# Kernel optimization log

Measured on AMD Instinct MI355X. Metric: run time of the kernel, lower is better.

The kernel has to match this reference:

```python
import jax, jax.numpy as jnp
import numpy as np

THRESHOLD = 0.01


def setup_inputs() -> dict:
    key = jax.random.key(0)
    ks = jax.random.split(key, 6)
    N = 100_000      # neurons (square connectome)
    NNZ = 6_400_000  # edges, avg degree 64
    B = 8            # batch
    T = 8            # num_layers / timesteps
    S = 5_000        # sensory neurons
    G = 200          # neuron-type groups
    rows = jax.random.randint(ks[0], (NNZ,), 0, N, dtype=jnp.int32)
    cols = jax.random.randint(ks[1], (NNZ,), 0, N, dtype=jnp.int32)
    vals = jax.random.normal(ks[2], (NNZ,), jnp.float32) * 0.05
    sensory_indices = jnp.arange(S, dtype=jnp.int32)
    group_indices = jax.random.randint(ks[3], (N,), 0, G, dtype=jnp.int32)
    slope = jnp.full((G,), 5.0, jnp.float32)       # tanh_steepness default
    raw_biases = jnp.zeros((G,), jnp.float32)      # default_bias = 0.0
    inputs = jax.random.uniform(ks[4], (B, S, T), jnp.float32)
    return dict(vals=vals, rows=rows, cols=cols, sensory_indices=sensory_indices,
                group_indices=group_indices, slope=slope, raw_biases=raw_biases,
                inputs=inputs, num_neurons=N)


def _spmm(vals, rows, cols, x, n):
    # y[i, b] = sum_e vals[e] * x[cols[e], b]   (COO sparse @ dense)
    return jax.ops.segment_sum(vals[:, None] * x[cols], rows, num_segments=n)


def reference(vals, rows, cols, sensory_indices, group_indices, slope,
              raw_biases, inputs, num_neurons):
    B, S, T = inputs.shape
    n = num_neurons
    # clip sensory inputs: below threshold -> 0, above 1 -> 1
    inputs = jnp.where(inputs >= THRESHOLD, inputs, 0.0)
    inputs = jnp.minimum(inputs, 1.0)
    slopes = slope[group_indices][:, None]                     # (N, 1)
    biases = jax.nn.softplus(raw_biases)[group_indices][:, None]

    def act(x):  # tanh(threshold(slope*x + bias))
        y = slopes * x + biases
        y = jnp.where(y >= THRESHOLD, y, 0.0)
        return jnp.tanh(y)

    acts = []
    # t = 0: only external input
    full = jnp.zeros((n, B), inputs.dtype).at[sensory_indices].add(inputs[:, :, 0].T)
    x = act(_spmm(vals, rows, cols, full, n))
    acts.append(x)
    # t >= 1: internal activation + external input
    for t in range(1, T):
        full = x.at[sensory_indices].add(inputs[:, :, t].T)
        x = act(_spmm(vals, rows, cols, full, n))
        acts.append(x)
    return jnp.stack(acts, axis=2).transpose(1, 0, 2)  # (B, N, T)
```

## Files before the change

kernel.cpp:

```cpp
#include <hip/hip_runtime.h>
#include <cstdint>
#include <cstddef>

constexpr int N       = 100000;
constexpr int NNZ     = 6400000;
constexpr int B       = 8;
constexpr int T       = 8;
constexpr int S       = 5000;
constexpr int BIN1_BITS = 8;
constexpr int BIN1    = 1 << BIN1_BITS;
constexpr int NBINS1  = (N + BIN1 - 1) / BIN1;
constexpr int CHUNK   = 8192;
constexpr int NCHUNKS = (NNZ + CHUNK - 1) / CHUNK;
constexpr int STAGE_CAP = 17408;
constexpr float THRESH = 0.01f;

__device__ __forceinline__ unsigned pack_val15(unsigned fbits, unsigned col17) {
    unsigned xb = fbits + 0x1000u;
    unsigned sign = xb >> 31;
    int ex = (int)((xb >> 23) & 0xFFu) - 110;
    ex = ex < 0 ? 0 : (ex > 15 ? 15 : ex);
    unsigned u15 = (sign << 14) | ((unsigned)ex << 10) | ((xb >> 13) & 0x3FFu);
    return (col17 << 15) | u15;
}

__device__ __forceinline__ float dec_val15(unsigned w) {
    unsigned fb = ((w & 0x4000u) << 17) | ((((w >> 10) & 0xFu) + 110u) << 23)
                | ((w & 0x3FFu) << 13);
    return __uint_as_float(fb);
}

__global__ void k_precompute_sb(const int* __restrict__ gi,
                                const float* __restrict__ slope,
                                const float* __restrict__ raw_biases,
                                float* __restrict__ slopeN,
                                float* __restrict__ biasN) {
    int i = blockIdx.x * 256 + threadIdx.x;
    if (i < N) {
        int g = gi[i];
        slopeN[i] = slope[g];
        float rb = raw_biases[g];
        biasN[i] = (rb > 20.0f) ? rb : log1pf(expf(rb));
    }
}

__global__ void k_hist(const int* __restrict__ rows, unsigned* __restrict__ counts) {
    __shared__ unsigned hist[NBINS1];
    int tid = threadIdx.x, chunk = blockIdx.x;
    for (int i = tid; i < NBINS1; i += 256) hist[i] = 0;
    __syncthreads();
    int base = chunk * CHUNK;
    #pragma unroll 4
    for (int it = 0; it < CHUNK / 256; ++it) {
        int e = base + it * 256 + tid;
        if (e < NNZ) atomicAdd(&hist[((unsigned)rows[e]) >> BIN1_BITS], 1u);
    }
    __syncthreads();
    for (int i = tid; i < NBINS1; i += 256) counts[(size_t)i * NCHUNKS + chunk] = hist[i];
}

__global__ void k_scan_chunks(unsigned* __restrict__ counts, unsigned* __restrict__ binTot) {
    int bin = blockIdx.x, lane = threadIdx.x;
    unsigned carry = 0;
    for (int bse = 0; bse < NCHUNKS; bse += 64) {
        int idx = bse + lane;
        unsigned v = (idx < NCHUNKS) ? counts[(size_t)bin * NCHUNKS + idx] : 0u;
        unsigned x = v;
        #pragma unroll
        for (int off = 1; off < 64; off <<= 1) {
            unsigned y = __shfl_up(x, off, 64);
            if (lane >= off) x += y;
        }
        if (idx < NCHUNKS) counts[(size_t)bin * NCHUNKS + idx] = x - v + carry;
        carry += __shfl(x, 63, 64);
    }
    if (lane == 0) binTot[bin] = carry;
}

__global__ void k_scan_bins(const unsigned* __restrict__ binTot, unsigned* __restrict__ binBase) {
    int lane = threadIdx.x;
    unsigned carry = 0;
    for (int bse = 0; bse < NBINS1; bse += 64) {
        int idx = bse + lane;
        unsigned v = (idx < NBINS1) ? binTot[idx] : 0u;
        unsigned x = v;
        #pragma unroll
        for (int off = 1; off < 64; off <<= 1) {
            unsigned y = __shfl_up(x, off, 64);
            if (lane >= off) x += y;
        }
        if (idx < NBINS1) binBase[idx] = x - v + carry;
        carry += __shfl(x, 63, 64);
    }
    if (lane == 0) binBase[NBINS1] = carry;
}

__global__ __launch_bounds__(512)
void k_scatter(const int* __restrict__ rows, const int* __restrict__ cols,
               const float* __restrict__ vals,
               const unsigned* __restrict__ binBase,
               const unsigned* __restrict__ counts,
               uint2* __restrict__ pk) {
    __shared__ uint2    stage[CHUNK];
    __shared__ unsigned lcnt[NBINS1];
    __shared__ unsigned lofs[NBINS1 + 1];
    __shared__ unsigned gdst[NBINS1];
    int tid = threadIdx.x, chunk = blockIdx.x;
    int base = chunk * CHUNK;
    for (int i = tid; i < NBINS1; i += 512) lcnt[i] = 0;
    __syncthreads();
    for (int i = tid; i < CHUNK; i += 512) {
        int e = base + i;
        if (e < NNZ) atomicAdd(&lcnt[((unsigned)rows[e]) >> BIN1_BITS], 1u);
    }
    __syncthreads();
    if (tid < 64) {
        unsigned carry = 0;
        for (int bse = 0; bse < NBINS1; bse += 64) {
            int idx = bse + tid;
            unsigned v = (idx < NBINS1) ? lcnt[idx] : 0u;
            unsigned x = v;
            #pragma unroll
            for (int off = 1; off < 64; off <<= 1) {
                unsigned y = __shfl_up(x, off, 64);
                if (tid >= off) x += y;
            }
            if (idx < NBINS1) lofs[idx] = x - v + carry;
            carry += __shfl(x, 63, 64);
        }
        if (tid == 0) lofs[NBINS1] = carry;
    }
    __syncthreads();
    if (tid < NBINS1) {
        lcnt[tid] = lofs[tid];
        gdst[tid] = binBase[tid] + counts[(size_t)tid * NCHUNKS + chunk];
    }
    __syncthreads();
    for (int i = tid; i < CHUNK; i += 512) {
        int e = base + i;
        if (e < NNZ) {
            unsigned r = (unsigned)rows[e];
            unsigned c = (unsigned)cols[e];
            float    v = vals[e];
            unsigned b1 = r >> BIN1_BITS, lr = r & (BIN1 - 1);
            unsigned pos = atomicAdd(&lcnt[b1], 1u);
            stage[pos] = make_uint2(__float_as_uint(v), c | (lr << 17));
        }
    }
    __syncthreads();
    int wave = tid >> 6, lane = tid & 63;
    for (int b1 = wave; b1 < NBINS1; b1 += 8) {
        unsigned s = lofs[b1], epos = lcnt[b1];
        unsigned g = gdst[b1];
        for (unsigned j = s + lane; j < epos; j += 64)
            pk[(size_t)g + (j - s)] = stage[j];
    }
}

__global__ __launch_bounds__(512)
void k_sortbin(const uint2* __restrict__ pk,
               const unsigned* __restrict__ binBase,
               unsigned* __restrict__ pk2,
               unsigned* __restrict__ rowPtr) {
    __shared__ unsigned stage[STAGE_CAP];
    __shared__ unsigned cnt[BIN1];
    __shared__ unsigned ofs[BIN1];
    int tid = threadIdx.x, bin = blockIdx.x;
    if (tid < BIN1) cnt[tid] = 0;
    __syncthreads();
    unsigned s = binBase[bin], e = binBase[bin + 1];
    unsigned total = e - s;
    for (unsigned i = s + tid; i < e; i += 512)
        atomicAdd(&cnt[pk[i].y >> 17], 1u);
    __syncthreads();
    if (tid < BIN1) ofs[tid] = cnt[tid];
    __syncthreads();
    for (int off = 1; off < BIN1; off <<= 1) {
        unsigned v = (tid < BIN1 && tid >= off) ? ofs[tid - off] : 0u;
        __syncthreads();
        if (tid < BIN1) ofs[tid] += v;
        __syncthreads();
    }
    if (tid < BIN1) {
        unsigned excl = ofs[tid] - cnt[tid];
        int row = bin * BIN1 + tid;
        if (row <= N) rowPtr[row] = s + excl;
        cnt[tid] = excl;
    }
    __syncthreads();
    if (total <= (unsigned)STAGE_CAP) {
        for (unsigned i = s + tid; i < e; i += 512) {
            uint2 p = pk[i];
            unsigned w = pack_val15(p.x, p.y & 0x1FFFFu);
            unsigned pos = atomicAdd(&cnt[p.y >> 17], 1u);
            stage[pos] = w;
        }
        __syncthreads();
        for (unsigned j = tid; j < total; j += 512)
            pk2[(size_t)s + j] = stage[j];
    } else {
        for (unsigned i = s + tid; i < e; i += 512) {
            uint2 p = pk[i];
            unsigned w = pack_val15(p.x, p.y & 0x1FFFFu);
            unsigned pos = atomicAdd(&cnt[p.y >> 17], 1u);
            pk2[(size_t)s + pos] = w;
        }
    }
}

__global__ void k_sensory(const float* __restrict__ inputs, const int* __restrict__ sidx,
                          float* __restrict__ X, int t) {
    int idx = blockIdx.x * 256 + threadIdx.x;
    if (idx < S * B) {
        int s = idx >> 3, b = idx & 7;
        float val = inputs[((size_t)b * S + s) * T + t];
        val = (val >= THRESH) ? fminf(val, 1.0f) : 0.0f;
        atomicAdd(&X[(size_t)sidx[s] * B + b], val);
    }
}

__device__ __forceinline__ float wave_fold8(const float* a, int lane) {
    int l1 = lane & 1, l2 = lane & 2, l4 = lane & 4;
    float k0 = l1 ? a[1] : a[0], s0 = l1 ? a[0] : a[1];
    float k1 = l1 ? a[3] : a[2], s1 = l1 ? a[2] : a[3];
    float k2 = l1 ? a[5] : a[4], s2 = l1 ? a[4] : a[5];
    float k3 = l1 ? a[7] : a[6], s3 = l1 ? a[6] : a[7];
    k0 += __shfl_xor(s0, 1, 64);
    k1 += __shfl_xor(s1, 1, 64);
    k2 += __shfl_xor(s2, 1, 64);
    k3 += __shfl_xor(s3, 1, 64);
    float m0 = l2 ? k1 : k0, t0 = l2 ? k0 : k1;
    float m1 = l2 ? k3 : k2, t1 = l2 ? k2 : k3;
    m0 += __shfl_xor(t0, 2, 64);
    m1 += __shfl_xor(t1, 2, 64);
    float r = l4 ? m1 : m0, u = l4 ? m0 : m1;
    r += __shfl_xor(u, 4, 64);
    r += __shfl_xor(r, 8, 64);
    r += __shfl_xor(r, 16, 64);
    r += __shfl_xor(r, 32, 64);
    return r;
}

__global__ __launch_bounds__(256)
void k_step(const unsigned* __restrict__ pk2,
            const unsigned* __restrict__ rowPtr,
            const float* __restrict__ Xin,
            const float* __restrict__ slopeN,
            const float* __restrict__ biasN,
            float* __restrict__ Sout,
            float* __restrict__ Xnext,
            const float* __restrict__ inputs, int tnext, int has_next, unsigned cmax) {
    int lane = threadIdx.x & 63;
    int wv = __builtin_amdgcn_readfirstlane(blockIdx.x * 4 + (threadIdx.x >> 6));
    int r0 = wv * 4;
    if (r0 >= N) return;

    unsigned P[5];
    #pragma unroll
    for (int r = 0; r < 5; ++r) {
        int rr = r0 + r; rr = rr > N ? N : rr;
        P[r] = rowPtr[rr];
    }

    float acc[4][8];
    #pragma unroll
    for (int r = 0; r < 4; ++r)
        #pragma unroll
        for (int b = 0; b < 8; ++b) acc[r][b] = 0.f;

    unsigned w1[4], w2[4];
    bool m1[4], m2[4];
    #pragma unroll
    for (int r = 0; r < 4; ++r) {
        unsigned e = P[r] + lane;
        m1[r] = e < P[r + 1];
        w1[r] = m1[r] ? pk2[e] : 0u;
    }
    #pragma unroll
    for (int r = 0; r < 4; ++r) {
        unsigned e = P[r] + 64 + lane;
        m2[r] = e < P[r + 1];
        w2[r] = m2[r] ? pk2[e] : 0u;
    }

    #pragma unroll
    for (int it = 0; it < 2; ++it) {
        #pragma unroll
        for (int r = 0; r < 4; ++r) {
            unsigned w = it ? w2[r] : w1[r];
            bool     m = it ? m2[r] : m1[r];
            float4 x0 = make_float4(0.f, 0.f, 0.f, 0.f), x1 = x0;
            if (m && (w >> 15) < cmax) {
                const float4* fx = (const float4*)(Xin + (size_t)(w >> 15) * B);
                x0 = fx[0]; x1 = fx[1];
            }
            float v = dec_val15(w);
            acc[r][0] += v * x0.x; acc[r][1] += v * x0.y;
            acc[r][2] += v * x0.z; acc[r][3] += v * x0.w;
            acc[r][4] += v * x1.x; acc[r][5] += v * x1.y;
            acc[r][6] += v * x1.z; acc[r][7] += v * x1.w;
        }
    }

    #pragma unroll
    for (int r = 0; r < 4; ++r) {
        for (unsigned e = P[r] + 128 + lane; e < P[r + 1]; e += 64) {
            unsigned w = pk2[e];
            float4 x0 = make_float4(0.f, 0.f, 0.f, 0.f), x1 = x0;
            if ((w >> 15) < cmax) {
                const float4* fx = (const float4*)(Xin + (size_t)(w >> 15) * B);
                x0 = fx[0]; x1 = fx[1];
            }
            float v = dec_val15(w);
            acc[r][0] += v * x0.x; acc[r][1] += v * x0.y;
            acc[r][2] += v * x0.z; acc[r][3] += v * x0.w;
            acc[r][4] += v * x1.x; acc[r][5] += v * x1.y;
            acc[r][6] += v * x1.z; acc[r][7] += v * x1.w;
        }
    }

    float f0 = wave_fold8(acc[0], lane);
    float f1 = wave_fold8(acc[1], lane);
    float f2 = wave_fold8(acc[2], lane);
    float f3 = wave_fold8(acc[3], lane);

    int lr = (lane >> 3) & 3;
    int b  = lane & 7;
    int row = r0 + lr;
    int rc = row < N - 1 ? row : N - 1;
    float sl = slopeN[rc], bi = biasN[rc];
    float fs = lr == 0 ? f0 : lr == 1 ? f1 : lr == 2 ? f2 : f3;
    float y = sl * fs + bi;
    y = (y >= THRESH) ? y : 0.f;
    float o = tanhf(y);

    if (lane < 32 && row < N) {
        size_t idx = (size_t)row * B + b;
        Sout[idx] = o;
        float xn = o;
        if (has_next && row < S) {
            float val = inputs[((size_t)b * S + row) * T + tnext];
            val = (val >= THRESH) ? fminf(val, 1.0f) : 0.0f;
            xn += val;
        }
        Xnext[idx] = xn;
    }
}

__global__ __launch_bounds__(512)
void k_transpose(const float* __restrict__ St, float* __restrict__ out) {
    __shared__ float tile[64][8][9];
    int r0 = blockIdx.x * 64;
    int tid = threadIdx.x;
    int ri = tid >> 3, rb = tid & 7;
    #pragma unroll
    for (int t = 0; t < T; ++t) {
        int r = r0 + ri;
        if (r < N)
            tile[ri][t][rb] = St[(size_t)t * N * B + (size_t)r * B + rb];
    }
    __syncthreads();
    int wi = tid >> 3, wt = tid & 7;
    #pragma unroll
    for (int b = 0; b < B; ++b) {
        int r = r0 + wi;
        if (r < N)
            out[(size_t)b * N * T + (size_t)r * T + wt] = tile[wi][wt][b];
    }
}

extern "C" void kernel_launch(void* const* d_in, const int* in_sizes, int n_in,
                              void* d_out, int out_size, void* d_ws, size_t ws_size,
                              hipStream_t stream) {
    const float* vals  = (const float*)d_in[0];
    const int*   rows  = (const int*)d_in[1];
    const int*   cols  = (const int*)d_in[2];
    const int*   sidx  = (const int*)d_in[3];
    const int*   gi    = (const int*)d_in[4];
    const float* slope = (const float*)d_in[5];
    const float* rawb  = (const float*)d_in[6];
    const float* inputs = (const float*)d_in[7];
    float* out = (float*)d_out;

    char* ws = (char*)d_ws;
    uint2*    pk     = (uint2*)ws;
    float*    St     = (float*)ws;
    float*    Xin0   = (float*)(ws + 25600000);
    float*    Xin1   = (float*)(ws + 28800000);
    float*    slopeN = (float*)(ws + 32000000);
    float*    biasN  = (float*)(ws + 32400000);
    char*     wsB    = ws + 51200000;
    unsigned* pk2    = (unsigned*)wsB;
    unsigned* counts = (unsigned*)wsB;
    char*     wsC    = wsB + 25600000;
    unsigned* binTot  = (unsigned*)(wsC);
    unsigned* binBase = (unsigned*)(wsC + 4096);
    unsigned* rowPtr  = (unsigned*)(wsC + 8192);
    size_t need = 76800000 + 8192 + (size_t)(N + 1) * 4 + 256;
    if (need > ws_size) return;

    k_hist<<<NCHUNKS, 256, 0, stream>>>(rows, counts);
    k_scan_chunks<<<NBINS1, 64, 0, stream>>>(counts, binTot);
    k_scan_bins<<<1, 64, 0, stream>>>(binTot, binBase);
    k_scatter<<<NCHUNKS, 512, 0, stream>>>(rows, cols, vals, binBase, counts, pk);
    k_sortbin<<<NBINS1, 512, 0, stream>>>(pk, binBase, pk2, rowPtr);
    k_precompute_sb<<<(N + 255) / 256, 256, 0, stream>>>(gi, slope, rawb, slopeN, biasN);

    hipMemsetAsync(Xin0, 0, (size_t)N * B * 4, stream);
    k_sensory<<<(S * B + 255) / 256, 256, 0, stream>>>(inputs, sidx, Xin0, 0);

    float* Xcur = Xin0;
    float* Xnxt = Xin1;
    for (int t = 0; t < T; ++t) {
        unsigned cmax = (t == 0) ? (unsigned)S : (unsigned)N;
        k_step<<<(N + 15) / 16, 256, 0, stream>>>(
            pk2, rowPtr, Xcur, slopeN, biasN, St + (size_t)t * N * B, Xnxt,
            inputs, t + 1, (t + 1 < T) ? 1 : 0, cmax);
        float* tmp = Xcur; Xcur = Xnxt; Xnxt = tmp;
    }
    k_transpose<<<(N + 63) / 64, 512, 0, stream>>>(St, out);
}
```

Measured before the change: 403.4 us.

## Vectorize COO preprocessing loads, reuse histogram counts in scatter, flatten copy-out

Halves the chunk size, uses int4/float4 loads in both the histogram and scatter kernels, and gives each wave its own shared-memory histogram copy to cut atomic contention. The scatter kernel no longer re-counts rows. It derives per-chunk bin counts from the exclusive-scanned counts array (next chunk minus current, or binTot for the last chunk). The staged copy-out now runs as a flat loop driven by a per-entry bin index, replacing the per-wave bin loop that left lanes idle on small bins. The trade-off is twice as many blocks and more scan work over NCHUNKS, plus extra shared memory for the bin-index array.

```diff
diff --git a/kernel.cpp b/kernel.cpp
--- a/kernel.cpp
+++ b/kernel.cpp
@@ -10,7 +10,7 @@
 constexpr int BIN1_BITS = 8;
 constexpr int BIN1    = 1 << BIN1_BITS;
 constexpr int NBINS1  = (N + BIN1 - 1) / BIN1;
-constexpr int CHUNK   = 8192;
+constexpr int CHUNK   = 4096;
 constexpr int NCHUNKS = (NNZ + CHUNK - 1) / CHUNK;
 constexpr int STAGE_CAP = 17408;
 constexpr float THRESH = 0.01f;
@@ -44,19 +44,29 @@
     }
 }
 
-__global__ void k_hist(const int* __restrict__ rows, unsigned* __restrict__ counts) {
-    __shared__ unsigned hist[NBINS1];
+__global__ __launch_bounds__(256)
+void k_hist(const int* __restrict__ rows, unsigned* __restrict__ counts) {
+    __shared__ unsigned hist[4][NBINS1];
     int tid = threadIdx.x, chunk = blockIdx.x;
-    for (int i = tid; i < NBINS1; i += 256) hist[i] = 0;
-    __syncthreads();
-    int base = chunk * CHUNK;
-    #pragma unroll 4
-    for (int it = 0; it < CHUNK / 256; ++it) {
-        int e = base + it * 256 + tid;
-        if (e < NNZ) atomicAdd(&hist[((unsigned)rows[e]) >> BIN1_BITS], 1u);
-    }
-    __syncthreads();
-    for (int i = tid; i < NBINS1; i += 256) counts[(size_t)i * NCHUNKS + chunk] = hist[i];
+    int wv = tid >> 6;
+    for (int i = tid; i < 4 * NBINS1; i += 256) ((unsigned*)hist)[i] = 0;
+    __syncthreads();
+    int base4 = chunk * (CHUNK / 4);
+    #pragma unroll
+    for (int it = 0; it < CHUNK / 1024; ++it) {
+        int i4 = base4 + it * 256 + tid;
+        if (i4 * 4 < NNZ) {
+            int4 r4 = ((const int4*)rows)[i4];
+            atomicAdd(&hist[wv][((unsigned)r4.x) >> BIN1_BITS], 1u);
+            atomicAdd(&hist[wv][((unsigned)r4.y) >> BIN1_BITS], 1u);
+            atomicAdd(&hist[wv][((unsigned)r4.z) >> BIN1_BITS], 1u);
+            atomicAdd(&hist[wv][((unsigned)r4.w) >> BIN1_BITS], 1u);
+        }
+    }
+    __syncthreads();
+    for (int i = tid; i < NBINS1; i += 256)
+        counts[(size_t)i * NCHUNKS + chunk] =
+            hist[0][i] + hist[1][i] + hist[2][i] + hist[3][i];
 }
 
 __global__ void k_scan_chunks(unsigned* __restrict__ counts, unsigned* __restrict__ binTot) {
@@ -99,19 +109,23 @@
 void k_scatter(const int* __restrict__ rows, const int* __restrict__ cols,
                const float* __restrict__ vals,
                const unsigned* __restrict__ binBase,
+               const unsigned* __restrict__ binTot,
                const unsigned* __restrict__ counts,
                uint2* __restrict__ pk) {
-    __shared__ uint2    stage[CHUNK];
+    __shared__ uint2          stage[CHUNK];
+    __shared__ unsigned short bidx[CHUNK];
     __shared__ unsigned lcnt[NBINS1];
     __shared__ unsigned lofs[NBINS1 + 1];
     __shared__ unsigned gdst[NBINS1];
     int tid = threadIdx.x, chunk = blockIdx.x;
     int base = chunk * CHUNK;
-    for (int i = tid; i < NBINS1; i += 512) lcnt[i] = 0;
-    __syncthreads();
-    for (int i = tid; i < CHUNK; i += 512) {
-        int e = base + i;
-        if (e < NNZ) atomicAdd(&lcnt[((unsigned)rows[e]) >> BIN1_BITS], 1u);
+
+    for (int i = tid; i < NBINS1; i += 512) {
+        unsigned cur = counts[(size_t)i * NCHUNKS + chunk];
+        unsigned nxt = (chunk + 1 < NCHUNKS) ? counts[(size_t)i * NCHUNKS + chunk + 1]
+                                             : binTot[i];
+        lcnt[i] = nxt - cur;
+        gdst[i] = binBase[i] + cur;
     }
     __syncthreads();
     if (tid < 64) {
@@ -131,29 +145,51 @@
         if (tid == 0) lofs[NBINS1] = carry;
     }
     __syncthreads();
-    if (tid < NBINS1) {
-        lcnt[tid] = lofs[tid];
-        gdst[tid] = binBase[tid] + counts[(size_t)tid * NCHUNKS + chunk];
-    }
-    __syncthreads();
-    for (int i = tid; i < CHUNK; i += 512) {
-        int e = base + i;
-        if (e < NNZ) {
-            unsigned r = (unsigned)rows[e];
-            unsigned c = (unsigned)cols[e];
-            float    v = vals[e];
-            unsigned b1 = r >> BIN1_BITS, lr = r & (BIN1 - 1);
-            unsigned pos = atomicAdd(&lcnt[b1], 1u);
-            stage[pos] = make_uint2(__float_as_uint(v), c | (lr << 17));
-        }
-    }
-    __syncthreads();
-    int wave = tid >> 6, lane = tid & 63;
-    for (int b1 = wave; b1 < NBINS1; b1 += 8) {
-        unsigned s = lofs[b1], epos = lcnt[b1];
-        unsigned g = gdst[b1];
-        for (unsigned j = s + lane; j < epos; j += 64)
-            pk[(size_t)g + (j - s)] = stage[j];
+    if (tid < NBINS1) lcnt[tid] = lofs[tid];
+    __syncthreads();
+
+    #pragma unroll
+    for (int it = 0; it < CHUNK / 2048; ++it) {
+        int i4 = base / 4 + it * 512 + tid;
+        if (i4 * 4 < NNZ) {
+            int4   r4 = ((const int4*)rows)[i4];
+            int4   c4 = ((const int4*)cols)[i4];
+            float4 v4 = ((const float4*)vals)[i4];
+            {
+                unsigned r = (unsigned)r4.x, b1 = r >> BIN1_BITS;
+                unsigned pos = atomicAdd(&lcnt[b1], 1u);
+                stage[pos] = make_uint2(__float_as_uint(v4.x),
+                                        (unsigned)c4.x | ((r & (BIN1 - 1)) << 17));
+                bidx[pos] = (unsigned short)b1;
+            }
+            {
+                unsigned r = (unsigned)r4.y, b1 = r >> BIN1_BITS;
+                unsigned pos = atomicAdd(&lcnt[b1], 1u);
+                stage[pos] = make_uint2(__float_as_uint(v4.y),
+                                        (unsigned)c4.y | ((r & (BIN1 - 1)) << 17));
+                bidx[pos] = (unsigned short)b1;
+            }
+            {
+                unsigned r = (unsigned)r4.z, b1 = r >> BIN1_BITS;
+                unsigned pos = atomicAdd(&lcnt[b1], 1u);
+                stage[pos] = make_uint2(__float_as_uint(v4.z),
+                                        (unsigned)c4.z | ((r & (BIN1 - 1)) << 17));
+                bidx[pos] = (unsigned short)b1;
+            }
+            {
+                unsigned r = (unsigned)r4.w, b1 = r >> BIN1_BITS;
+                unsigned pos = atomicAdd(&lcnt[b1], 1u);
+                stage[pos] = make_uint2(__float_as_uint(v4.w),
+                                        (unsigned)c4.w | ((r & (BIN1 - 1)) << 17));
+                bidx[pos] = (unsigned short)b1;
+            }
+        }
+    }
+    __syncthreads();
+    unsigned total = lofs[NBINS1];
+    for (unsigned j = tid; j < total; j += 512) {
+        unsigned b = bidx[j];
+        pk[(size_t)gdst[b] + (j - lofs[b])] = stage[j];
     }
 }
 
@@ -402,7 +438,7 @@
     k_hist<<<NCHUNKS, 256, 0, stream>>>(rows, counts);
     k_scan_chunks<<<NBINS1, 64, 0, stream>>>(counts, binTot);
     k_scan_bins<<<1, 64, 0, stream>>>(binTot, binBase);
-    k_scatter<<<NCHUNKS, 512, 0, stream>>>(rows, cols, vals, binBase, counts, pk);
+    k_scatter<<<NCHUNKS, 512, 0, stream>>>(rows, cols, vals, binBase, binTot, counts, pk);
     k_sortbin<<<NBINS1, 512, 0, stream>>>(pk, binBase, pk2, rowPtr);
     k_precompute_sb<<<(N + 255) / 256, 256, 0, stream>>>(gi, slope, rawb, slopeN, biasN);
 
```

Measured after the change: 392.9 us (median of 2 runs). 1.03x faster.

## Replace two-pass binned COO-to-CSR sort with direct per-row atomic histogram and scatter

Applied to the files above, without the earlier changes.

Replaces the chunked bin histogram, shared-memory staging scatter and per-bin local sort with a global per-row atomic histogram, a three-kernel prefix scan, and a direct atomic-cursor scatter into packed CSR. This removes the intermediate 8-byte staging array and several passes over it. In exchange it issues millions of global atomics at random addresses, and it writes scattered 4-byte values, which makes the order of entries within a row nondeterministic.

```diff
diff --git a/kernel.cpp b/kernel.cpp
--- a/kernel.cpp
+++ b/kernel.cpp
@@ -7,12 +7,8 @@
 constexpr int B       = 8;
 constexpr int T       = 8;
 constexpr int S       = 5000;
-constexpr int BIN1_BITS = 8;
-constexpr int BIN1    = 1 << BIN1_BITS;
-constexpr int NBINS1  = (N + BIN1 - 1) / BIN1;
-constexpr int CHUNK   = 8192;
-constexpr int NCHUNKS = (NNZ + CHUNK - 1) / CHUNK;
-constexpr int STAGE_CAP = 17408;
+constexpr int SCAN_BT = 1024;
+constexpr int SCAN_NB = (N + SCAN_BT - 1) / SCAN_BT;
 constexpr float THRESH = 0.01f;
 
 __device__ __forceinline__ unsigned pack_val15(unsigned fbits, unsigned col17) {
@@ -44,167 +40,100 @@
     }
 }
 
-__global__ void k_hist(const int* __restrict__ rows, unsigned* __restrict__ counts) {
-    __shared__ unsigned hist[NBINS1];
-    int tid = threadIdx.x, chunk = blockIdx.x;
-    for (int i = tid; i < NBINS1; i += 256) hist[i] = 0;
+__global__ __launch_bounds__(256)
+void k_hist_row(const int* __restrict__ rows, unsigned* __restrict__ rowCnt) {
+    int i4 = blockIdx.x * 256 + threadIdx.x;
+    if (i4 * 4 < NNZ) {
+        int4 r4 = ((const int4*)rows)[i4];
+        atomicAdd(&rowCnt[(unsigned)r4.x], 1u);
+        atomicAdd(&rowCnt[(unsigned)r4.y], 1u);
+        atomicAdd(&rowCnt[(unsigned)r4.z], 1u);
+        atomicAdd(&rowCnt[(unsigned)r4.w], 1u);
+    }
+}
+
+__global__ __launch_bounds__(1024)
+void k_scanA(const unsigned* __restrict__ rowCnt, unsigned* __restrict__ rowPtr,
+             unsigned* __restrict__ blockSum) {
+    __shared__ unsigned wsum[16];
+    int tid = threadIdx.x;
+    int idx = blockIdx.x * SCAN_BT + tid;
+    unsigned v = (idx < N) ? rowCnt[idx] : 0u;
+    unsigned x = v;
+    #pragma unroll
+    for (int off = 1; off < 64; off <<= 1) {
+        unsigned y = __shfl_up(x, off, 64);
+        if ((tid & 63) >= off) x += y;
+    }
+    int wv = tid >> 6, ln = tid & 63;
+    if (ln == 63) wsum[wv] = x;
     __syncthreads();
-    int base = chunk * CHUNK;
-    #pragma unroll 4
-    for (int it = 0; it < CHUNK / 256; ++it) {
-        int e = base + it * 256 + tid;
-        if (e < NNZ) atomicAdd(&hist[((unsigned)rows[e]) >> BIN1_BITS], 1u);
+    if (tid < 16) {
+        unsigned s = wsum[tid];
+        unsigned y = s;
+        #pragma unroll
+        for (int off = 1; off < 16; off <<= 1) {
+            unsigned z = __shfl_up(y, off, 64);
+            if (tid >= off) y += z;
+        }
+        wsum[tid] = y - s;
     }
     __syncthreads();
-    for (int i = tid; i < NBINS1; i += 256) counts[(size_t)i * NCHUNKS + chunk] = hist[i];
-}
-
-__global__ void k_scan_chunks(unsigned* __restrict__ counts, unsigned* __restrict__ binTot) {
-    int bin = blockIdx.x, lane = threadIdx.x;
+    unsigned excl = x - v + wsum[wv];
+    if (idx < N) rowPtr[idx] = excl;
+    if (tid == SCAN_BT - 1) blockSum[blockIdx.x] = wsum[15] + x;
+}
+
+__global__ void k_scanB(unsigned* __restrict__ blockSum) {
+    int lane = threadIdx.x;
     unsigned carry = 0;
-    for (int bse = 0; bse < NCHUNKS; bse += 64) {
+    for (int bse = 0; bse < SCAN_NB; bse += 64) {
         int idx = bse + lane;
-        unsigned v = (idx < NCHUNKS) ? counts[(size_t)bin * NCHUNKS + idx] : 0u;
+        unsigned v = (idx < SCAN_NB) ? blockSum[idx] : 0u;
         unsigned x = v;
         #pragma unroll
         for (int off = 1; off < 64; off <<= 1) {
             unsigned y = __shfl_up(x, off, 64);
             if (lane >= off) x += y;
         }
-        if (idx < NCHUNKS) counts[(size_t)bin * NCHUNKS + idx] = x - v + carry;
+        if (idx < SCAN_NB) blockSum[idx] = x - v + carry;
         carry += __shfl(x, 63, 64);
     }
-    if (lane == 0) binTot[bin] = carry;
-}
-
-__global__ void k_scan_bins(const unsigned* __restrict__ binTot, unsigned* __restrict__ binBase) {
-    int lane = threadIdx.x;
-    unsigned carry = 0;
-    for (int bse = 0; bse < NBINS1; bse += 64) {
-        int idx = bse + lane;
-        unsigned v = (idx < NBINS1) ? binTot[idx] : 0u;
-        unsigned x = v;
-        #pragma unroll
-        for (int off = 1; off < 64; off <<= 1) {
-            unsigned y = __shfl_up(x, off, 64);
-            if (lane >= off) x += y;
-        }
-        if (idx < NBINS1) binBase[idx] = x - v + carry;
-        carry += __shfl(x, 63, 64);
-    }
-    if (lane == 0) binBase[NBINS1] = carry;
-}
-
-__global__ __launch_bounds__(512)
-void k_scatter(const int* __restrict__ rows, const int* __restrict__ cols,
-               const float* __restrict__ vals,
-               const unsigned* __restrict__ binBase,
-               const unsigned* __restrict__ counts,
-               uint2* __restrict__ pk) {
-    __shared__ uint2    stage[CHUNK];
-    __shared__ unsigned lcnt[NBINS1];
-    __shared__ unsigned lofs[NBINS1 + 1];
-    __shared__ unsigned gdst[NBINS1];
-    int tid = threadIdx.x, chunk = blockIdx.x;
-    int base = chunk * CHUNK;
-    for (int i = tid; i < NBINS1; i += 512) lcnt[i] = 0;
-    __syncthreads();
-    for (int i = tid; i < CHUNK; i += 512) {
-        int e = base + i;
-        if (e < NNZ) atomicAdd(&lcnt[((unsigned)rows[e]) >> BIN1_BITS], 1u);
-    }
-    __syncthreads();
-    if (tid < 64) {
-        unsigned carry = 0;
-        for (int bse = 0; bse < NBINS1; bse += 64) {
-            int idx = bse + tid;
-            unsigned v = (idx < NBINS1) ? lcnt[idx] : 0u;
-            unsigned x = v;
-            #pragma unroll
-            for (int off = 1; off < 64; off <<= 1) {
-                unsigned y = __shfl_up(x, off, 64);
-                if (tid >= off) x += y;
-            }
-            if (idx < NBINS1) lofs[idx] = x - v + carry;
-            carry += __shfl(x, 63, 64);
-        }
-        if (tid == 0) lofs[NBINS1] = carry;
-    }
-    __syncthreads();
-    if (tid < NBINS1) {
-        lcnt[tid] = lofs[tid];
-        gdst[tid] = binBase[tid] + counts[(size_t)tid * NCHUNKS + chunk];
-    }
-    __syncthreads();
-    for (int i = tid; i < CHUNK; i += 512) {
-        int e = base + i;
-        if (e < NNZ) {
-            unsigned r = (unsigned)rows[e];
-            unsigned c = (unsigned)cols[e];
-            float    v = vals[e];
-            unsigned b1 = r >> BIN1_BITS, lr = r & (BIN1 - 1);
-            unsigned pos = atomicAdd(&lcnt[b1], 1u);
-            stage[pos] = make_uint2(__float_as_uint(v), c | (lr << 17));
-        }
-    }
-    __syncthreads();
-    int wave = tid >> 6, lane = tid & 63;
-    for (int b1 = wave; b1 < NBINS1; b1 += 8) {
-        unsigned s = lofs[b1], epos = lcnt[b1];
-        unsigned g = gdst[b1];
-        for (unsigned j = s + lane; j < epos; j += 64)
-            pk[(size_t)g + (j - s)] = stage[j];
-    }
-}
-
-__global__ __launch_bounds__(512)
-void k_sortbin(const uint2* __restrict__ pk,
-               const unsigned* __restrict__ binBase,
-               unsigned* __restrict__ pk2,
-               unsigned* __restrict__ rowPtr) {
-    __shared__ unsigned stage[STAGE_CAP];
-    __shared__ unsigned cnt[BIN1];
-    __shared__ unsigned ofs[BIN1];
-    int tid = threadIdx.x, bin = blockIdx.x;
-    if (tid < BIN1) cnt[tid] = 0;
-    __syncthreads();
-    unsigned s = binBase[bin], e = binBase[bin + 1];
-    unsigned total = e - s;
-    for (unsigned i = s + tid; i < e; i += 512)
-        atomicAdd(&cnt[pk[i].y >> 17], 1u);
-    __syncthreads();
-    if (tid < BIN1) ofs[tid] = cnt[tid];
-    __syncthreads();
-    for (int off = 1; off < BIN1; off <<= 1) {
-        unsigned v = (tid < BIN1 && tid >= off) ? ofs[tid - off] : 0u;
-        __syncthreads();
-        if (tid < BIN1) ofs[tid] += v;
-        __syncthreads();
-    }
-    if (tid < BIN1) {
-        unsigned excl = ofs[tid] - cnt[tid];
-        int row = bin * BIN1 + tid;
-        if (row <= N) rowPtr[row] = s + excl;
-        cnt[tid] = excl;
-    }
-    __syncthreads();
-    if (total <= (unsigned)STAGE_CAP) {
-        for (unsigned i = s + tid; i < e; i += 512) {
-            uint2 p = pk[i];
-            unsigned w = pack_val15(p.x, p.y & 0x1FFFFu);
-            unsigned pos = atomicAdd(&cnt[p.y >> 17], 1u);
-            stage[pos] = w;
-        }
-        __syncthreads();
-        for (unsigned j = tid; j < total; j += 512)
-            pk2[(size_t)s + j] = stage[j];
-    } else {
-        for (unsigned i = s + tid; i < e; i += 512) {
-            uint2 p = pk[i];
-            unsigned w = pack_val15(p.x, p.y & 0x1FFFFu);
-            unsigned pos = atomicAdd(&cnt[p.y >> 17], 1u);
-            pk2[(size_t)s + pos] = w;
-        }
+}
+
+__global__ __launch_bounds__(1024)
+void k_scanC(unsigned* __restrict__ rowPtr, const unsigned* __restrict__ blockSum,
+             unsigned* __restrict__ cursors) {
+    int idx = blockIdx.x * SCAN_BT + threadIdx.x;
+    if (idx < N) {
+        unsigned p = rowPtr[idx] + blockSum[blockIdx.x];
+        rowPtr[idx]  = p;
+        cursors[idx] = p;
+    }
+    if (idx == N) rowPtr[N] = NNZ;
+}
+
+__global__ __launch_bounds__(256)
+void k_scatter_direct(const int* __restrict__ rows, const int* __restrict__ cols,
+                      const float* __restrict__ vals,
+                      unsigned* __restrict__ cursors, unsigned* __restrict__ pk2) {
+    int i4 = blockIdx.x * 256 + threadIdx.x;
+    if (i4 * 4 < NNZ) {
+        int4   r4 = ((const int4*)rows)[i4];
+        int4   c4 = ((const int4*)cols)[i4];
+        float4 v4 = ((const float4*)vals)[i4];
+        unsigned w0 = pack_val15(__float_as_uint(v4.x), (unsigned)c4.x);
+        unsigned w1 = pack_val15(__float_as_uint(v4.y), (unsigned)c4.y);
+        unsigned w2 = pack_val15(__float_as_uint(v4.z), (unsigned)c4.z);
+        unsigned w3 = pack_val15(__float_as_uint(v4.w), (unsigned)c4.w);
+        unsigned p0 = atomicAdd(&cursors[(unsigned)r4.x], 1u);
+        unsigned p1 = atomicAdd(&cursors[(unsigned)r4.y], 1u);
+        unsigned p2 = atomicAdd(&cursors[(unsigned)r4.z], 1u);
+        unsigned p3 = atomicAdd(&cursors[(unsigned)r4.w], 1u);
+        pk2[p0] = w0;
+        pk2[p1] = w1;
+        pk2[p2] = w2;
+        pk2[p3] = w3;
     }
 }
 
@@ -383,27 +312,26 @@
     float* out = (float*)d_out;
 
     char* ws = (char*)d_ws;
-    uint2*    pk     = (uint2*)ws;
-    float*    St     = (float*)ws;
-    float*    Xin0   = (float*)(ws + 25600000);
-    float*    Xin1   = (float*)(ws + 28800000);
-    float*    slopeN = (float*)(ws + 32000000);
-    float*    biasN  = (float*)(ws + 32400000);
-    char*     wsB    = ws + 51200000;
-    unsigned* pk2    = (unsigned*)wsB;
-    unsigned* counts = (unsigned*)wsB;
-    char*     wsC    = wsB + 25600000;
-    unsigned* binTot  = (unsigned*)(wsC);
-    unsigned* binBase = (unsigned*)(wsC + 4096);
-    unsigned* rowPtr  = (unsigned*)(wsC + 8192);
-    size_t need = 76800000 + 8192 + (size_t)(N + 1) * 4 + 256;
+    float*    St      = (float*)ws;
+    float*    Xin0    = (float*)(ws + 25600000);
+    float*    Xin1    = (float*)(ws + 28800000);
+    float*    slopeN  = (float*)(ws + 32000000);
+    float*    biasN   = (float*)(ws + 32400000);
+    unsigned* pk2     = (unsigned*)(ws + 51200000);
+    unsigned* rowCnt  = (unsigned*)(ws + 76800000);
+    unsigned* rowPtr  = (unsigned*)(ws + 77300000);
+    unsigned* cursors = (unsigned*)(ws + 77800000);
+    unsigned* blockSum= (unsigned*)(ws + 78300000);
+    size_t need = 78300000 + 4096;
     if (need > ws_size) return;
 
-    k_hist<<<NCHUNKS, 256, 0, stream>>>(rows, counts);
-    k_scan_chunks<<<NBINS1, 64, 0, stream>>>(counts, binTot);
-    k_scan_bins<<<1, 64, 0, stream>>>(binTot, binBase);
-    k_scatter<<<NCHUNKS, 512, 0, stream>>>(rows, cols, vals, binBase, counts, pk);
-    k_sortbin<<<NBINS1, 512, 0, stream>>>(pk, binBase, pk2, rowPtr);
+    hipMemsetAsync(rowCnt, 0, (size_t)N * 4, stream);
+    k_hist_row<<<NNZ / 4 / 256, 256, 0, stream>>>(rows, rowCnt);
+    k_scanA<<<SCAN_NB, SCAN_BT, 0, stream>>>(rowCnt, rowPtr, blockSum);
+    k_scanB<<<1, 64, 0, stream>>>(blockSum);
+    k_scanC<<<SCAN_NB, SCAN_BT, 0, stream>>>(rowPtr, blockSum, cursors);
+    k_scatter_direct<<<NNZ / 4 / 256, 256, 0, stream>>>(rows, cols, vals, cursors, pk2);
+
     k_precompute_sb<<<(N + 255) / 256, 256, 0, stream>>>(gi, slope, rawb, slopeN, biasN);
 
     hipMemsetAsync(Xin0, 0, (size_t)N * B * 4, stream);
```

Result: slower. 1.034 ms (+156.4%).
